# Kernel tuning notes

Measured on AMD Instinct MI355X. Metric: run time of the kernel, lower is better.

## Reference

```python
import jax, jax.numpy as jnp
import numpy as np

N_A, N_G, D, H = 100000, 25000, 128, 4
E_B, E_O, E_R, E_P = 400000, 100000, 200000, 200000
BN_INV = float(1.0 / np.sqrt(1.0 + 1e-5))  # eval-mode BatchNorm1d, running mean 0 / var 1


def setup_inputs():
    key = jax.random.key(0)
    ks = iter(jax.random.split(key, 64))
    nrm = lambda shape, s=0.05: jax.random.normal(next(ks), shape, jnp.float32) * s
    ri = lambda n, hi: jax.random.randint(next(ks), (n,), 0, hi, jnp.int32)
    inp = dict(
        x_atom=nrm((N_A, D), 1.0), x_group=nrm((N_G, D), 1.0),
        ef_bond=nrm((E_B, D), 1.0), ef_overlap=nrm((E_O, D), 1.0),
        bond_src=ri(E_B, N_A), bond_dst=ri(E_B, N_A),
        ov_src=ri(E_O, N_G), ov_dst=ri(E_O, N_G),
        ref_src=ri(E_R, N_G), ref_dst=ri(E_R, N_A),
        pool_src=ri(E_P, N_A), pool_dst=ri(E_P, N_G),
    )
    # two GINE convs (bond 'b', overlap 'o'): eps + MLP Linear(D,2D)->BN->ReLU->Linear(2D,D)
    for pre in ('b', 'o'):
        inp[pre + '_eps'] = jnp.zeros((1,), jnp.float32)
        inp[pre + '_W1'] = nrm((D, 2 * D)); inp[pre + '_b1'] = jnp.zeros((2 * D,), jnp.float32)
        inp[pre + '_g1'] = jnp.ones((2 * D,), jnp.float32); inp[pre + '_be1'] = jnp.zeros((2 * D,), jnp.float32)
        inp[pre + '_W2'] = nrm((2 * D, D)); inp[pre + '_b2'] = jnp.zeros((D,), jnp.float32)
    # two ModifiedGATConvs (refine 'r', pool 'p'): GATConv + Flatten->BN->ReLU->Linear
    for pre in ('r', 'p'):
        inp[pre + '_Wfc'] = nrm((D, H * D)); inp[pre + '_al'] = nrm((H, D)); inp[pre + '_ar'] = nrm((H, D))
        inp[pre + '_Wres'] = nrm((D, H * D)); inp[pre + '_bias'] = jnp.zeros((H * D,), jnp.float32)
        inp[pre + '_g'] = jnp.ones((H * D,), jnp.float32); inp[pre + '_b'] = jnp.zeros((H * D,), jnp.float32)
        inp[pre + '_Wout'] = nrm((H * D, D)); inp[pre + '_bout'] = jnp.zeros((D,), jnp.float32)
    return inp


def _gine(x_src, x_dst, efeat, src, dst, n_dst, eps, W1, b1, g1, be1, W2, b2):
    m = jax.nn.relu(x_src[src] + efeat)                       # [E, D] message: relu(h_src + e)
    neigh = jax.ops.segment_sum(m, dst, num_segments=n_dst)   # [Nd, D] sum-reduce
    h = (1.0 + eps) * x_dst + neigh
    h = h @ W1 + b1
    h = jax.nn.relu(g1 * (h * BN_INV) + be1)                  # eval BN
    return h @ W2 + b2


def _gat(x_src, x_dst, src, dst, n_dst, Wfc, al, ar, Wres, bias, g, b, Wout, bout):
    hs = (x_src @ Wfc).reshape(-1, H, D)                      # [Ns, H, D]
    hd = (x_dst @ Wfc).reshape(-1, H, D)
    el = jnp.sum(hs * al, axis=-1)                            # [Ns, H]
    er = jnp.sum(hd * ar, axis=-1)                            # [Nd, H]
    e = jax.nn.leaky_relu(el[src] + er[dst], 0.2)             # [E, H]
    emax = jax.ops.segment_max(e, dst, num_segments=n_dst)    # per-dst softmax (stable)
    ex = jnp.exp(e - emax[dst])
    den = jax.ops.segment_sum(ex, dst, num_segments=n_dst)
    a = ex / jnp.maximum(den[dst], 1e-9)                      # [E, H]
    rst = jax.ops.segment_sum(a[:, :, None] * hs[src], dst, num_segments=n_dst)  # [Nd, H, D]
    rst = rst + (x_dst @ Wres).reshape(-1, H, D) + bias.reshape(H, D)            # residual + bias
    flat = rst.reshape(-1, H * D)                             # Flatten
    h = jax.nn.relu(g * (flat * BN_INV) + b)                  # eval BN -> ReLU
    return h @ Wout + bout


def reference(x_atom, x_group, ef_bond, ef_overlap, bond_src, bond_dst, ov_src, ov_dst, ref_src, ref_dst, pool_src, pool_dst, b_eps, b_W1, b_b1, b_g1, b_be1, b_W2, b_b2, o_eps, o_W1, o_b1, o_g1, o_be1, o_W2, o_b2, r_Wfc, r_al, r_ar, r_Wres, r_bias, r_g, r_b, r_Wout, r_bout, p_Wfc, p_al, p_ar, p_Wres, p_bias, p_g, p_b, p_Wout, p_bout):
    # HeteroGraphConv with default 'sum' cross-relation aggregation per dst node type
    out_atom = _gine(x_atom, x_atom, ef_bond, bond_src, bond_dst, N_A, b_eps, b_W1, b_b1, b_g1, b_be1, b_W2, b_b2)
    out_atom = out_atom + _gat(x_group, x_atom, ref_src, ref_dst, N_A, r_Wfc, r_al, r_ar, r_Wres, r_bias, r_g, r_b, r_Wout, r_bout)
    out_group = _gine(x_group, x_group, ef_overlap, ov_src, ov_dst, N_G, o_eps, o_W1, o_b1, o_g1, o_be1, o_W2, o_b2)
    out_group = out_group + _gat(x_atom, x_group, pool_src, pool_dst, N_G, p_Wfc, p_al, p_ar, p_Wres, p_bias, p_g, p_b, p_Wout, p_bout)
    return jnp.concatenate([out_atom, out_group], axis=0)     # [N_A + N_G, D]
```

## Files before the change

### kernel.cpp

```cpp
#include <hip/hip_runtime.h>
#include <hip/hip_bf16.h>

#define N_A 100000
#define N_G 25000
#define DD 128
#define E_B 400000
#define E_O 100000
#define E_R 200000
#define E_P 200000
#define CAP 256

static constexpr float BN_INV_C = 0.99999500003749969f;

typedef __attribute__((ext_vector_type(8))) short bf16x8;
typedef __attribute__((ext_vector_type(4))) float f32x4;

__device__ __forceinline__ unsigned short f2bf(float f) {
    unsigned u = __float_as_uint(f);
    unsigned r = (u + 0x7FFFu + ((u >> 16) & 1u)) >> 16;
    return (unsigned short)r;
}
__device__ __forceinline__ float bf2f(unsigned short s) {
    return __uint_as_float(((unsigned)s) << 16);
}
__device__ __forceinline__ float lrelu(float v) { return v > 0.f ? v : 0.2f * v; }

__global__ void k_xcast_all(const float* __restrict__ xa, const float* __restrict__ xg,
                            unsigned short* __restrict__ xab, unsigned short* __restrict__ xgb) {
    int t = blockIdx.x * blockDim.x + threadIdx.x;
    if (t < N_A * 32) {
        float4 v = *(const float4*)(xa + (size_t)t * 4);
        ushort4 o; o.x = f2bf(v.x); o.y = f2bf(v.y); o.z = f2bf(v.z); o.w = f2bf(v.w);
        *(ushort4*)(xab + (size_t)t * 4) = o;
    } else {
        int t2 = t - N_A * 32;
        if (t2 >= N_G * 32) return;
        float4 v = *(const float4*)(xg + (size_t)t2 * 4);
        ushort4 o; o.x = f2bf(v.x); o.y = f2bf(v.y); o.z = f2bf(v.z); o.w = f2bf(v.w);
        *(ushort4*)(xgb + (size_t)t2 * 4) = o;
    }
}

struct WcSeg { const float* src; unsigned short* dst; int K; int N; int ldk; int off; };
struct WcArgs { WcSeg s[10]; };

__global__ void k_wcast_all(WcArgs a) {
    WcSeg sg = a.s[blockIdx.y];
    int t = blockIdx.x * blockDim.x + threadIdx.x;
    if (t >= sg.K * sg.N) return;
    int n = t % sg.N, k = t / sg.N;
    sg.dst[(size_t)n * sg.ldk + sg.off + k] = f2bf(sg.src[t]);
}

__global__ void k_war_all(const float* __restrict__ rWfc, const float* __restrict__ ral,
                          const float* __restrict__ rar, const float* __restrict__ pWfc,
                          const float* __restrict__ pal, const float* __restrict__ par,
                          float* __restrict__ wv) {
    int bsel = blockIdx.x;
    const float* W = bsel < 2 ? rWfc : pWfc;
    const float* vec = bsel == 0 ? ral : bsel == 1 ? rar : bsel == 2 ? pal : par;
    float* o = wv + bsel * 512;
    int t = threadIdx.x;
    int k = t >> 2, h = t & 3;
    const float* wr = W + (size_t)k * 512 + h * 128;
    const float* av = vec + h * 128;
    float s = 0.f;
    for (int d = 0; d < 128; ++d) s += wr[d] * av[d];
    o[t] = s;
}

__global__ void k_ll_build_all(const int* __restrict__ bd, const int* __restrict__ od,
                               const int* __restrict__ rd, const int* __restrict__ pd,
                               int* __restrict__ heads, int* __restrict__ nxt) {
    int t = blockIdx.x * blockDim.x + threadIdx.x;
    if (t < E_B) {
        nxt[t] = atomicExch(&heads[bd[t]], t);
    } else if (t < E_B + E_O) {
        int e = t - E_B;
        nxt[E_B + e] = atomicExch(&heads[100000 + od[e]], e);
    } else if (t < E_B + E_O + E_R) {
        int e = t - E_B - E_O;
        nxt[E_B + E_O + e] = atomicExch(&heads[125000 + rd[e]], e);
    } else if (t < E_B + E_O + E_R + E_P) {
        int e = t - E_B - E_O - E_R;
        nxt[E_B + E_O + E_R + e] = atomicExch(&heads[225000 + pd[e]], e);
    }
}

__global__ __launch_bounds__(64) void k_gine_gather_all(
    const unsigned short* __restrict__ xAb, const unsigned short* __restrict__ xGb,
    const float* __restrict__ efB, const float* __restrict__ efO,
    const int* __restrict__ bsrc, const int* __restrict__ osrc,
    const int* __restrict__ heads, const int* __restrict__ nxt,
    const float* __restrict__ beps, const float* __restrict__ oeps,
    unsigned short* __restrict__ h0A, unsigned short* __restrict__ h0G) {
    int n = blockIdx.x, lane = threadIdx.x;
    const unsigned short* xs; const unsigned short* xdrow; const float* ef;
    const int* esrc; const int* hd; const int* nx; float ep; unsigned short* outp; int nn;
    if (n < N_A) {
        nn = n; xs = xAb; xdrow = xAb + (size_t)n * DD; ef = efB; esrc = bsrc;
        hd = heads; nx = nxt; ep = 1.0f + beps[0]; outp = h0A + (size_t)n * DD;
    } else {
        nn = n - N_A; xs = xGb; xdrow = xGb + (size_t)nn * DD; ef = efO; esrc = osrc;
        hd = heads + 100000; nx = nxt + E_B; ep = 1.0f + oeps[0]; outp = h0G + (size_t)nn * DD;
    }
    float2 acc = make_float2(0.f, 0.f);
    for (int e = hd[nn]; e >= 0; e = nx[e]) {
        int s = esrc[e];
        unsigned xa = *(const unsigned*)(xs + (size_t)s * DD + lane * 2);
        float2 ev = *(const float2*)(ef + (size_t)e * DD + lane * 2);
        acc.x += fmaxf(bf2f((unsigned short)(xa & 0xffff)) + ev.x, 0.f);
        acc.y += fmaxf(bf2f((unsigned short)(xa >> 16)) + ev.y, 0.f);
    }
    unsigned xd = *(const unsigned*)(xdrow + lane * 2);
    float rx = ep * bf2f((unsigned short)(xd & 0xffff)) + acc.x;
    float ry = ep * bf2f((unsigned short)(xd >> 16)) + acc.y;
    *(unsigned*)(outp + lane * 2) = (unsigned)f2bf(rx) | ((unsigned)f2bf(ry) << 16);
}

__global__ void k_el_all(const unsigned short* __restrict__ xAb,
                         const unsigned short* __restrict__ xGb,
                         const float* __restrict__ wv,
                         float* __restrict__ elR, float* __restrict__ elP) {
    int t = blockIdx.x * blockDim.x + threadIdx.x;
    const unsigned short* xr; const float* wvp; float* op; int idx;
    if (t < N_G * 4) {
        idx = t; xr = xGb + (size_t)(t >> 2) * DD; wvp = wv; op = elR;
    } else {
        int t2 = t - N_G * 4;
        if (t2 >= N_A * 4) return;
        idx = t2; xr = xAb + (size_t)(t2 >> 2) * DD; wvp = wv + 1024; op = elP;
    }
    int h = idx & 3;
    float s = 0.f;
#pragma unroll
    for (int k = 0; k < DD; k += 8) {
        uint4 w = *(const uint4*)(xr + k);
        unsigned wa[4] = {w.x, w.y, w.z, w.w};
#pragma unroll
        for (int q = 0; q < 4; ++q) {
            s += bf2f((unsigned short)(wa[q] & 0xffff)) * wvp[(k + q * 2) * 4 + h];
            s += bf2f((unsigned short)(wa[q] >> 16)) * wvp[(k + q * 2 + 1) * 4 + h];
        }
    }
    op[idx] = s;
}

__global__ __launch_bounds__(64) void k_att_gather_all(
    const unsigned short* __restrict__ xAb, const unsigned short* __restrict__ xGb,
    const float* __restrict__ elR, const float* __restrict__ elP,
    const float* __restrict__ wv,
    const int* __restrict__ rsrc, const int* __restrict__ psrc,
    const int* __restrict__ heads, const int* __restrict__ nxt,
    unsigned short* __restrict__ A2r, unsigned short* __restrict__ A2p) {
    int n = blockIdx.x, lane = threadIdx.x;
    const unsigned short* xs; const unsigned short* xdrow; const float* el;
    const float* wvr; const int* esrc; const int* hd; const int* nx;
    unsigned short* A2; int nn;
    if (n < N_A) {
        nn = n; xs = xGb; xdrow = xAb + (size_t)n * DD; el = elR; wvr = wv + 512;
        esrc = rsrc; hd = heads + 125000; nx = nxt + (E_B + E_O);
        A2 = A2r + (size_t)n * 512;
    } else {
        nn = n - N_A; xs = xAb; xdrow = xGb + (size_t)nn * DD; el = elP; wvr = wv + 1536;
        esrc = psrc; hd = heads + 225000; nx = nxt + (E_B + E_O + E_R);
        A2 = A2p + (size_t)nn * 512;
    }
    __shared__ int elist[CAP];
    unsigned xd = *(const unsigned*)(xdrow + lane * 2);
    float xd0 = bf2f((unsigned short)(xd & 0xffff));
    float xd1 = bf2f((unsigned short)(xd >> 16));
    float er[4];
#pragma unroll
    for (int h = 0; h < 4; ++h)
        er[h] = xd0 * wvr[(2 * lane) * 4 + h] + xd1 * wvr[(2 * lane + 1) * 4 + h];
#pragma unroll
    for (int m = 1; m < 64; m <<= 1) {
#pragma unroll
        for (int h = 0; h < 4; ++h) er[h] += __shfl_xor(er[h], m, 64);
    }
    float mx[4] = {-1e30f, -1e30f, -1e30f, -1e30f};
    int cnt = 0, erest = -1;
    for (int e = hd[nn]; e >= 0; e = nx[e]) {
        int s = esrc[e];
        float4 e4 = *(const float4*)(el + (size_t)s * 4);
        mx[0] = fmaxf(mx[0], lrelu(e4.x + er[0]));
        mx[1] = fmaxf(mx[1], lrelu(e4.y + er[1]));
        mx[2] = fmaxf(mx[2], lrelu(e4.z + er[2]));
        mx[3] = fmaxf(mx[3], lrelu(e4.w + er[3]));
        if (cnt < CAP) {
            if (lane == 0) elist[cnt] = e;
            cnt++;
        } else if (erest < 0) {
            erest = e;
        }
    }
    __syncthreads();
    float den[4] = {0.f, 0.f, 0.f, 0.f};
    for (int i = 0; i < cnt; ++i) {
        int s = esrc[elist[i]];
        float4 e4 = *(const float4*)(el + (size_t)s * 4);
        den[0] += __expf(lrelu(e4.x + er[0]) - mx[0]);
        den[1] += __expf(lrelu(e4.y + er[1]) - mx[1]);
        den[2] += __expf(lrelu(e4.z + er[2]) - mx[2]);
        den[3] += __expf(lrelu(e4.w + er[3]) - mx[3]);
    }
    for (int e = erest; e >= 0; e = nx[e]) {
        int s = esrc[e];
        float4 e4 = *(const float4*)(el + (size_t)s * 4);
        den[0] += __expf(lrelu(e4.x + er[0]) - mx[0]);
        den[1] += __expf(lrelu(e4.y + er[1]) - mx[1]);
        den[2] += __expf(lrelu(e4.z + er[2]) - mx[2]);
        den[3] += __expf(lrelu(e4.w + er[3]) - mx[3]);
    }
    float inv[4];
#pragma unroll
    for (int h = 0; h < 4; ++h) inv[h] = 1.f / fmaxf(den[h], 1e-9f);
    float acc[4][2] = {};
    for (int i = 0; i < cnt; ++i) {
        int s = esrc[elist[i]];
        float4 e4 = *(const float4*)(el + (size_t)s * 4);
        unsigned xw = *(const unsigned*)(xs + (size_t)s * DD + lane * 2);
        float x0 = bf2f((unsigned short)(xw & 0xffff));
        float x1 = bf2f((unsigned short)(xw >> 16));
        float a0 = __expf(lrelu(e4.x + er[0]) - mx[0]) * inv[0];
        float a1 = __expf(lrelu(e4.y + er[1]) - mx[1]) * inv[1];
        float a2 = __expf(lrelu(e4.z + er[2]) - mx[2]) * inv[2];
        float a3 = __expf(lrelu(e4.w + er[3]) - mx[3]) * inv[3];
        acc[0][0] += a0 * x0; acc[0][1] += a0 * x1;
        acc[1][0] += a1 * x0; acc[1][1] += a1 * x1;
        acc[2][0] += a2 * x0; acc[2][1] += a2 * x1;
        acc[3][0] += a3 * x0; acc[3][1] += a3 * x1;
    }
    for (int e = erest; e >= 0; e = nx[e]) {
        int s = esrc[e];
        float4 e4 = *(const float4*)(el + (size_t)s * 4);
        unsigned xw = *(const unsigned*)(xs + (size_t)s * DD + lane * 2);
        float x0 = bf2f((unsigned short)(xw & 0xffff));
        float x1 = bf2f((unsigned short)(xw >> 16));
        float a0 = __expf(lrelu(e4.x + er[0]) - mx[0]) * inv[0];
        float a1 = __expf(lrelu(e4.y + er[1]) - mx[1]) * inv[1];
        float a2 = __expf(lrelu(e4.z + er[2]) - mx[2]) * inv[2];
        float a3 = __expf(lrelu(e4.w + er[3]) - mx[3]) * inv[3];
        acc[0][0] += a0 * x0; acc[0][1] += a0 * x1;
        acc[1][0] += a1 * x0; acc[1][1] += a1 * x1;
        acc[2][0] += a2 * x0; acc[2][1] += a2 * x1;
        acc[3][0] += a3 * x0; acc[3][1] += a3 * x1;
    }
#pragma unroll
    for (int h = 0; h < 4; ++h) {
        unsigned o = (unsigned)f2bf(acc[h][0]) | ((unsigned)f2bf(acc[h][1]) << 16);
        *(unsigned*)(A2 + h * 128 + lane * 2) = o;
    }
}

#define LDKP 40
template <int EPI, int OUTBF, int GATK>
__global__ __launch_bounds__(256) void k_gemm_bf(
    const unsigned short* __restrict__ A, const unsigned short* __restrict__ Bt,
    void* __restrict__ C, int M, int N, int K,
    const float* __restrict__ bias, const float* __restrict__ g,
    const float* __restrict__ be, const unsigned short* __restrict__ addbf,
    const unsigned short* __restrict__ Axd) {
    __shared__ unsigned short As[128 * LDKP];
    __shared__ unsigned short Bs[128 * LDKP];
    int tid = threadIdx.x;
    int wave = tid >> 6, lane = tid & 63;
    int wr = wave >> 1, wc = wave & 1;
    int row0 = blockIdx.y * 128, col0 = blockIdx.x * 128;
    int l16 = lane & 15, khalf = (lane >> 4) * 8;
    f32x4 acc[4][4] = {};
    int r_0 = tid >> 2, ko_0 = (tid & 3) * 8;
    int r_1 = (tid + 256) >> 2, ko_1 = ((tid + 256) & 3) * 8;
    for (int k0 = 0; k0 < K; k0 += 32) {
        __syncthreads();
        {
            int kk = k0 + ko_0;
            int ra = min(row0 + r_0, M - 1);
            uint4 va;
            if (GATK) va = (kk < 128) ? *(const uint4*)(A + (size_t)ra * 512 + col0 + kk)
                                      : *(const uint4*)(Axd + (size_t)ra * 128 + (kk - 128));
            else va = *(const uint4*)(A + (size_t)ra * K + kk);
            *(uint4*)(&As[r_0 * LDKP + ko_0]) = va;
            uint4 vb = *(const uint4*)(Bt + (size_t)(col0 + r_0) * K + kk);
            *(uint4*)(&Bs[r_0 * LDKP + ko_0]) = vb;
            kk = k0 + ko_1;
            ra = min(row0 + r_1, M - 1);
            if (GATK) va = (kk < 128) ? *(const uint4*)(A + (size_t)ra * 512 + col0 + kk)
                                      : *(const uint4*)(Axd + (size_t)ra * 128 + (kk - 128));
            else va = *(const uint4*)(A + (size_t)ra * K + kk);
            *(uint4*)(&As[r_1 * LDKP + ko_1]) = va;
            vb = *(const uint4*)(Bt + (size_t)(col0 + r_1) * K + kk);
            *(uint4*)(&Bs[r_1 * LDKP + ko_1]) = vb;
        }
        __syncthreads();
        bf16x8 af[4], bfr[4];
#pragma unroll
        for (int i = 0; i < 4; ++i)
            af[i] = *(const bf16x8*)(&As[(wr * 64 + i * 16 + l16) * LDKP + khalf]);
#pragma unroll
        for (int j = 0; j < 4; ++j)
            bfr[j] = *(const bf16x8*)(&Bs[(wc * 64 + j * 16 + l16) * LDKP + khalf]);
#pragma unroll
        for (int i = 0; i < 4; ++i)
#pragma unroll
            for (int j = 0; j < 4; ++j)
                acc[i][j] = __builtin_amdgcn_mfma_f32_16x16x32_bf16(af[i], bfr[j], acc[i][j], 0, 0, 0);
    }
    int rq = (lane >> 4) * 4;
#pragma unroll
    for (int i = 0; i < 4; ++i) {
#pragma unroll
        for (int reg = 0; reg < 4; ++reg) {
            int r = row0 + wr * 64 + i * 16 + rq + reg;
            if (r >= M) continue;
#pragma unroll
            for (int j = 0; j < 4; ++j) {
                int c = col0 + wc * 64 + j * 16 + l16;
                float v = acc[i][j][reg];
                size_t idx = (size_t)r * N + c;
                v += bias[c];
                if (EPI == 2) {
                    v = g[c] * (v * BN_INV_C) + be[c];
                    v = fmaxf(v, 0.f);
                }
                if (EPI == 3) {
                    ((float*)C)[idx] = v + bf2f(addbf[idx]);
                } else if (OUTBF) {
                    ((unsigned short*)C)[idx] = f2bf(v);
                } else {
                    ((float*)C)[idx] = v;
                }
            }
        }
    }
}

extern "C" void kernel_launch(void* const* d_in, const int* in_sizes, int n_in,
                              void* d_out, int out_size, void* d_ws, size_t ws_size,
                              hipStream_t stream) {
    const float* x_atom = (const float*)d_in[0];
    const float* x_group = (const float*)d_in[1];
    const float* ef_bond = (const float*)d_in[2];
    const float* ef_ov = (const float*)d_in[3];
    const int* bond_src = (const int*)d_in[4];
    const int* bond_dst = (const int*)d_in[5];
    const int* ov_src = (const int*)d_in[6];
    const int* ov_dst = (const int*)d_in[7];
    const int* ref_src = (const int*)d_in[8];
    const int* ref_dst = (const int*)d_in[9];
    const int* pool_src = (const int*)d_in[10];
    const int* pool_dst = (const int*)d_in[11];
    const float* b_eps = (const float*)d_in[12];
    const float* b_W1 = (const float*)d_in[13];
    const float* b_b1 = (const float*)d_in[14];
    const float* b_g1 = (const float*)d_in[15];
    const float* b_be1 = (const float*)d_in[16];
    const float* b_W2 = (const float*)d_in[17];
    const float* b_b2 = (const float*)d_in[18];
    const float* o_eps = (const float*)d_in[19];
    const float* o_W1 = (const float*)d_in[20];
    const float* o_b1 = (const float*)d_in[21];
    const float* o_g1 = (const float*)d_in[22];
    const float* o_be1 = (const float*)d_in[23];
    const float* o_W2 = (const float*)d_in[24];
    const float* o_b2 = (const float*)d_in[25];
    const float* r_Wfc = (const float*)d_in[26];
    const float* r_al = (const float*)d_in[27];
    const float* r_ar = (const float*)d_in[28];
    const float* r_Wres = (const float*)d_in[29];
    const float* r_bias = (const float*)d_in[30];
    const float* r_g = (const float*)d_in[31];
    const float* r_b = (const float*)d_in[32];
    const float* r_Wout = (const float*)d_in[33];
    const float* r_bout = (const float*)d_in[34];
    const float* p_Wfc = (const float*)d_in[35];
    const float* p_al = (const float*)d_in[36];
    const float* p_ar = (const float*)d_in[37];
    const float* p_Wres = (const float*)d_in[38];
    const float* p_bias = (const float*)d_in[39];
    const float* p_g = (const float*)d_in[40];
    const float* p_b = (const float*)d_in[41];
    const float* p_Wout = (const float*)d_in[42];
    const float* p_bout = (const float*)d_in[43];

    float* out = (float*)d_out;
    char* wsb = (char*)d_ws;
    unsigned short* xAb = (unsigned short*)(wsb + 0);
    unsigned short* xGb = (unsigned short*)(wsb + 26000000);
    unsigned short* WtB1 = (unsigned short*)(wsb + 33000000);
    unsigned short* WtB2 = WtB1 + 32768;
    unsigned short* WtO1 = WtB2 + 32768;
    unsigned short* WtO2 = WtO1 + 32768;
    unsigned short* WtR  = WtO2 + 32768;
    unsigned short* WtRo = WtR + 131072;
    unsigned short* WtP  = WtRo + 65536;
    unsigned short* WtPo = WtP + 131072;
    float* wv   = (float*)(wsb + 34100000);
    float* elR  = (float*)(wsb + 34200000);
    float* elP  = (float*)(wsb + 34600000);
    int* heads  = (int*)(wsb + 36300000);
    int* nxt    = (int*)(wsb + 37400000);
    unsigned short* h0A = (unsigned short*)(wsb + 41100000);
    unsigned short* h0G = (unsigned short*)(wsb + 66800000);
    unsigned short* R4  = (unsigned short*)(wsb + 73300000);
    unsigned short* G1a = (unsigned short*)(wsb + 124600000);
    unsigned short* G1g = (unsigned short*)(wsb + 150300000);
    unsigned short* A2r = (unsigned short*)(wsb + 156800000);
    unsigned short* A2p = (unsigned short*)(wsb + 259300000);
    unsigned short* R3r = (unsigned short*)(wsb + 285000000);
    unsigned short* R3p = (unsigned short*)(wsb + 387500000);

    k_xcast_all<<<((N_A + N_G) * 32 + 255) / 256, 256, 0, stream>>>(x_atom, x_group, xAb, xGb);
    WcArgs wa;
    wa.s[0] = {b_W1, WtB1, 128, 256, 128, 0};
    wa.s[1] = {b_W2, WtB2, 256, 128, 256, 0};
    wa.s[2] = {o_W1, WtO1, 128, 256, 128, 0};
    wa.s[3] = {o_W2, WtO2, 256, 128, 256, 0};
    wa.s[4] = {r_Wfc, WtR, 128, 512, 256, 0};
    wa.s[5] = {r_Wres, WtR, 128, 512, 256, 128};
    wa.s[6] = {r_Wout, WtRo, 512, 128, 512, 0};
    wa.s[7] = {p_Wfc, WtP, 128, 512, 256, 0};
    wa.s[8] = {p_Wres, WtP, 128, 512, 256, 128};
    wa.s[9] = {p_Wout, WtPo, 512, 128, 512, 0};
    k_wcast_all<<<dim3(256, 10), 256, 0, stream>>>(wa);
    k_war_all<<<4, 512, 0, stream>>>(r_Wfc, r_al, r_ar, p_Wfc, p_al, p_ar, wv);
    hipMemsetAsync(heads, 0xFF, 250000 * 4, stream);
    k_ll_build_all<<<(E_B + E_O + E_R + E_P + 255) / 256, 256, 0, stream>>>(
        bond_dst, ov_dst, ref_dst, pool_dst, heads, nxt);
    k_gine_gather_all<<<N_A + N_G, 64, 0, stream>>>(xAb, xGb, ef_bond, ef_ov, bond_src, ov_src,
                                                    heads, nxt, b_eps, o_eps, h0A, h0G);
    k_gemm_bf<2, 1, 0><<<dim3(2, 782), 256, 0, stream>>>(h0A, WtB1, R4, N_A, 256, 128, b_b1, b_g1, b_be1, nullptr, nullptr);
    k_gemm_bf<1, 1, 0><<<dim3(1, 782), 256, 0, stream>>>(R4, WtB2, G1a, N_A, 128, 256, b_b2, nullptr, nullptr, nullptr, nullptr);
    k_gemm_bf<2, 1, 0><<<dim3(2, 196), 256, 0, stream>>>(h0G, WtO1, R4, N_G, 256, 128, o_b1, o_g1, o_be1, nullptr, nullptr);
    k_gemm_bf<1, 1, 0><<<dim3(1, 196), 256, 0, stream>>>(R4, WtO2, G1g, N_G, 128, 256, o_b2, nullptr, nullptr, nullptr, nullptr);
    k_el_all<<<((N_G + N_A) * 4 + 255) / 256, 256, 0, stream>>>(xAb, xGb, wv, elR, elP);
    k_att_gather_all<<<N_A + N_G, 64, 0, stream>>>(xAb, xGb, elR, elP, wv, ref_src, pool_src,
                                                   heads, nxt, A2r, A2p);
    k_gemm_bf<2, 1, 1><<<dim3(4, 782), 256, 0, stream>>>(A2r, WtR, R3r, N_A, 512, 256, r_bias, r_g, r_b, nullptr, xAb);
    k_gemm_bf<2, 1, 1><<<dim3(4, 196), 256, 0, stream>>>(A2p, WtP, R3p, N_G, 512, 256, p_bias, p_g, p_b, nullptr, xGb);
    k_gemm_bf<3, 0, 0><<<dim3(1, 782), 256, 0, stream>>>(R3r, WtRo, out, N_A, 128, 512, r_bout, nullptr, nullptr, G1a, nullptr);
    k_gemm_bf<3, 0, 0><<<dim3(1, 196), 256, 0, stream>>>(R3p, WtPo, out + (size_t)N_A * DD, N_G, 128, 512, p_bout, nullptr, nullptr, G1g, nullptr);
}
```

Before: 618.2 us.

## Parallelize GAT edge softmax across lanes and cache scores in shared memory

The GAT aggregation kernel previously had every lane redundantly walk the edge list three times, reloading source indices and attention logits and recomputing exp each pass. The new code first collects source ids into shared memory, then splits logit, max and exp work across the 64 lanes with wave reductions. It stores the normalized-ready exponentials in shared memory so the weighted-sum pass only reads them. This adds shared memory per block and shuffle reductions. The overflow path beyond the edge cap still runs serially.

Result: no change. 609.3 us (-1.4%).

```diff
diff --git a/kernel.cpp b/kernel.cpp
--- a/kernel.cpp
+++ b/kernel.cpp
@@ -166,7 +166,8 @@
         esrc = psrc; hd = heads + 225000; nx = nxt + (E_B + E_O + E_R);
         A2 = A2p + (size_t)nn * 512;
     }
-    __shared__ int elist[CAP];
+    __shared__ int slist[CAP];
+    __shared__ float sa[4][CAP];
     unsigned xd = *(const unsigned*)(xdrow + lane * 2);
     float xd0 = bf2f((unsigned short)(xd & 0xffff));
     float xd1 = bf2f((unsigned short)(xd >> 16));
@@ -179,31 +180,55 @@
 #pragma unroll
         for (int h = 0; h < 4; ++h) er[h] += __shfl_xor(er[h], m, 64);
     }
-    float mx[4] = {-1e30f, -1e30f, -1e30f, -1e30f};
     int cnt = 0, erest = -1;
     for (int e = hd[nn]; e >= 0; e = nx[e]) {
+        if (cnt < CAP) {
+            if (lane == 0) slist[cnt] = esrc[e];
+            cnt++;
+        } else {
+            erest = e;
+            break;
+        }
+    }
+    __syncthreads();
+    float mx[4] = {-1e30f, -1e30f, -1e30f, -1e30f};
+    for (int i = lane; i < cnt; i += 64) {
+        int s = slist[i];
+        float4 e4 = *(const float4*)(el + (size_t)s * 4);
+        float l0 = lrelu(e4.x + er[0]);
+        float l1 = lrelu(e4.y + er[1]);
+        float l2 = lrelu(e4.z + er[2]);
+        float l3 = lrelu(e4.w + er[3]);
+        sa[0][i] = l0; sa[1][i] = l1; sa[2][i] = l2; sa[3][i] = l3;
+        mx[0] = fmaxf(mx[0], l0); mx[1] = fmaxf(mx[1], l1);
+        mx[2] = fmaxf(mx[2], l2); mx[3] = fmaxf(mx[3], l3);
+    }
+#pragma unroll
+    for (int m = 1; m < 64; m <<= 1) {
+#pragma unroll
+        for (int h = 0; h < 4; ++h) mx[h] = fmaxf(mx[h], __shfl_xor(mx[h], m, 64));
+    }
+    for (int e = erest; e >= 0; e = nx[e]) {
         int s = esrc[e];
         float4 e4 = *(const float4*)(el + (size_t)s * 4);
         mx[0] = fmaxf(mx[0], lrelu(e4.x + er[0]));
         mx[1] = fmaxf(mx[1], lrelu(e4.y + er[1]));
         mx[2] = fmaxf(mx[2], lrelu(e4.z + er[2]));
         mx[3] = fmaxf(mx[3], lrelu(e4.w + er[3]));
-        if (cnt < CAP) {
-            if (lane == 0) elist[cnt] = e;
-            cnt++;
-        } else if (erest < 0) {
-            erest = e;
-        }
-    }
-    __syncthreads();
+    }
     float den[4] = {0.f, 0.f, 0.f, 0.f};
-    for (int i = 0; i < cnt; ++i) {
-        int s = esrc[elist[i]];
-        float4 e4 = *(const float4*)(el + (size_t)s * 4);
-        den[0] += __expf(lrelu(e4.x + er[0]) - mx[0]);
-        den[1] += __expf(lrelu(e4.y + er[1]) - mx[1]);
-        den[2] += __expf(lrelu(e4.z + er[2]) - mx[2]);
-        den[3] += __expf(lrelu(e4.w + er[3]) - mx[3]);
+    for (int i = lane; i < cnt; i += 64) {
+        float v0 = __expf(sa[0][i] - mx[0]);
+        float v1 = __expf(sa[1][i] - mx[1]);
+        float v2 = __expf(sa[2][i] - mx[2]);
+        float v3 = __expf(sa[3][i] - mx[3]);
+        sa[0][i] = v0; sa[1][i] = v1; sa[2][i] = v2; sa[3][i] = v3;
+        den[0] += v0; den[1] += v1; den[2] += v2; den[3] += v3;
+    }
+#pragma unroll
+    for (int m = 1; m < 64; m <<= 1) {
+#pragma unroll
+        for (int h = 0; h < 4; ++h) den[h] += __shfl_xor(den[h], m, 64);
     }
     for (int e = erest; e >= 0; e = nx[e]) {
         int s = esrc[e];
@@ -216,17 +241,17 @@
     float inv[4];
 #pragma unroll
     for (int h = 0; h < 4; ++h) inv[h] = 1.f / fmaxf(den[h], 1e-9f);
+    __syncthreads();
     float acc[4][2] = {};
     for (int i = 0; i < cnt; ++i) {
-        int s = esrc[elist[i]];
-        float4 e4 = *(const float4*)(el + (size_t)s * 4);
+        int s = slist[i];
+        float a0 = sa[0][i] * inv[0];
+        float a1 = sa[1][i] * inv[1];
+        float a2 = sa[2][i] * inv[2];
+        float a3 = sa[3][i] * inv[3];
         unsigned xw = *(const unsigned*)(xs + (size_t)s * DD + lane * 2);
         float x0 = bf2f((unsigned short)(xw & 0xffff));
         float x1 = bf2f((unsigned short)(xw >> 16));
-        float a0 = __expf(lrelu(e4.x + er[0]) - mx[0]) * inv[0];
-        float a1 = __expf(lrelu(e4.y + er[1]) - mx[1]) * inv[1];
-        float a2 = __expf(lrelu(e4.z + er[2]) - mx[2]) * inv[2];
-        float a3 = __expf(lrelu(e4.w + er[3]) - mx[3]) * inv[3];
         acc[0][0] += a0 * x0; acc[0][1] += a0 * x1;
         acc[1][0] += a1 * x0; acc[1][1] += a1 * x1;
         acc[2][0] += a2 * x0; acc[2][1] += a2 * x1;
```
